# Optimization experiments

Measured on AMD Instinct MI355X. Metric: run time of the kernel, lower is better.

## Reference

```python
import jax, jax.numpy as jnp
import numpy as np

N_NODES = 100000
N_EDGES = 1600000
N_FEAT = 128
HID = 64


def setup_inputs() -> dict:
    key = jax.random.key(0)
    ks = jax.random.split(key, 8)
    s = 0.05
    return {
        "x": jax.random.normal(ks[0], (N_NODES, N_FEAT), jnp.float32),
        "edge_index": jax.random.randint(ks[1], (2, N_EDGES), 0, N_NODES, jnp.int64),
        "labels": jax.random.randint(ks[2], (N_NODES, 1), 0, 2, jnp.int32),
        "W1": jax.random.normal(ks[3], (N_FEAT, HID), jnp.float32) * s,
        "b1": jnp.zeros((HID,), jnp.float32),
        "W2": jax.random.normal(ks[4], (HID, HID), jnp.float32) * s,
        "b2": jnp.zeros((HID,), jnp.float32),
        "W3": jax.random.normal(ks[5], (HID, HID), jnp.float32) * s,
        "b3": jnp.zeros((HID,), jnp.float32),
        "lW1": jax.random.normal(ks[6], (HID, 8), jnp.float32) * s,
        "lb1": jnp.zeros((8,), jnp.float32),
        "lW2": jax.random.normal(ks[7], (8, 1), jnp.float32) * s,
        "lb2": jnp.zeros((1,), jnp.float32),
    }


def reference(x, edge_index, labels, W1, b1, W2, b2, W3, b3, lW1, lb1, lW2, lb2):
    n = x.shape[0]
    # PyG GCNConv: add self-loops, symmetric D^{-1/2}(A+I)D^{-1/2} normalization
    loop = jnp.arange(n)
    row = jnp.concatenate([edge_index[0], loop])  # sources
    col = jnp.concatenate([edge_index[1], loop])  # targets (aggregation)
    deg = jax.ops.segment_sum(jnp.ones(col.shape, x.dtype), col, num_segments=n)
    dinv = jax.lax.rsqrt(deg)  # deg >= 1 thanks to self loops
    norm = dinv[row] * dinv[col]  # [E+N]

    def gcn(h, W, b):
        m = (h @ W)[row] * norm[:, None]  # gather + scale per edge
        return jax.ops.segment_sum(m, col, num_segments=n) + b

    h = jax.nn.relu(gcn(x, W1, b1))   # dropout inactive in eval mode
    h = jax.nn.relu(gcn(h, W2, b2))
    h = jax.nn.relu(gcn(h, W3, b3))
    h = jax.nn.relu(h @ lW1 + lb1)
    p = jax.nn.sigmoid(h @ lW2 + lb2)  # [N,1]

    y = labels.astype(x.dtype)
    # generate_weights(labels): class-balance weights (minority class up-weighted)
    pm = jnp.mean(y)
    w = y * (1.0 - pm) + (1.0 - y) * pm
    eps = 1e-7
    pc = jnp.clip(p, eps, 1.0 - eps)
    bce = -(y * jnp.log(pc) + (1.0 - y) * jnp.log(1.0 - pc))
    loss = jnp.mean(w * bce)
    return loss, p
```

## Files before the change

### kernel.cpp

```cpp
#include <hip/hip_runtime.h>
#include <cstdint>
#include <cstddef>

typedef __attribute__((ext_vector_type(8))) short short8;
typedef __attribute__((ext_vector_type(4))) float f32x4;
typedef __attribute__((ext_vector_type(2))) float f32x2;

#define NBLK 512
#define NBLK_SHIFT 9

__device__ inline unsigned short f2bf(float f) {
  union { float f; unsigned int u; } x; x.f = f;
  unsigned int r = x.u + 0x7FFFu + ((x.u >> 16) & 1u);
  return (unsigned short)(r >> 16);
}
__device__ inline float bf2f(unsigned short s) {
  union { unsigned int u; float f; } x; x.u = ((unsigned int)s) << 16;
  return x.f;
}


__global__ __launch_bounds__(256) void hist_kernel(const int* __restrict__ cols,
                                                   int* __restrict__ histG,
                                                   const int* __restrict__ labels,
                                                   float* __restrict__ labelsum,
                                                   const float* __restrict__ W1,
                                                   const float* __restrict__ W2,
                                                   const float* __restrict__ W3,
                                                   unsigned short* __restrict__ Wt1,
                                                   unsigned short* __restrict__ Wt2,
                                                   unsigned short* __restrict__ Wt3,
                                                   int E, int N, int NBUCK) {
  __shared__ int h[512];
  if (blockIdx.x < 3) {
    const float* W; unsigned short* Wt; int K;
    if (blockIdx.x == 0)      { W = W1; Wt = Wt1; K = 128; }
    else if (blockIdx.x == 1) { W = W2; Wt = Wt2; K = 64; }
    else                      { W = W3; Wt = Wt3; K = 64; }
    int total = K * 64;
    for (int i = threadIdx.x; i < total; i += 256) {
      int n = i / K, k = i - n * K;
      Wt[i] = f2bf(W[k * 64 + n]);
    }
  }
  {
    int chunkL = (N + NBLK - 1) / NBLK;
    int ls = blockIdx.x * chunkL;
    int le = min(N, ls + chunkL);
    float v = 0.f;
    for (int i = ls + threadIdx.x; i < le; i += 256) v += (float)labels[i];
#pragma unroll
    for (int o = 32; o > 0; o >>= 1) v += __shfl_down(v, o);
    __shared__ float sl[4];
    if ((threadIdx.x & 63) == 0) sl[threadIdx.x >> 6] = v;
    __syncthreads();
    if (threadIdx.x == 0) labelsum[blockIdx.x] = sl[0] + sl[1] + sl[2] + sl[3];
  }
  for (int i = threadIdx.x; i < NBUCK; i += 256) h[i] = 0;
  __syncthreads();
  int chunk = (E + NBLK - 1) / NBLK;
  int s = blockIdx.x * chunk;
  int e = min(E, s + chunk);
  for (int i = s + threadIdx.x; i < e; i += 256) atomicAdd(&h[cols[i] >> 8], 1);
  __syncthreads();
  for (int i = threadIdx.x; i < NBUCK; i += 256)
    histG[blockIdx.x * NBUCK + i] = h[i];
}


__global__ __launch_bounds__(256) void scan_partials_t(const int* __restrict__ histG,
                                                       int* __restrict__ partials,
                                                       int total, int NBUCK) {
  int i = blockIdx.x * 256 + threadIdx.x;
  int v = 0;
  if (i < total) {
    int bucket = i >> NBLK_SHIFT, blk = i & (NBLK - 1);
    v = histG[blk * NBUCK + bucket];
  }
#pragma unroll
  for (int o = 32; o > 0; o >>= 1) v += __shfl_down(v, o);
  __shared__ int s[4];
  if ((threadIdx.x & 63) == 0) s[threadIdx.x >> 6] = v;
  __syncthreads();
  if (threadIdx.x == 0) partials[blockIdx.x] = s[0] + s[1] + s[2] + s[3];
}

__global__ __launch_bounds__(256) void scan_block(int* __restrict__ partials, int nb,
                                                  float* __restrict__ loss,
                                                  const float* __restrict__ labelsum,
                                                  float* __restrict__ pmsum) {
  __shared__ int tmp[256];
  __shared__ int carry;
  int tid = threadIdx.x;
  {
    float v = 0.f;
    for (int i = tid; i < NBLK; i += 256) v += labelsum[i];
#pragma unroll
    for (int o = 32; o > 0; o >>= 1) v += __shfl_down(v, o);
    __shared__ float sl[4];
    if ((tid & 63) == 0) sl[tid >> 6] = v;
    __syncthreads();
    if (tid == 0) *pmsum = sl[0] + sl[1] + sl[2] + sl[3];
  }
  if (tid == 0) { carry = 0; *loss = 0.f; }
  __syncthreads();
  for (int base = 0; base < nb; base += 256) {
    int i = base + tid;
    int v = (i < nb) ? partials[i] : 0;
    tmp[tid] = v;
    __syncthreads();
    int incl = v;
    for (int o = 1; o < 256; o <<= 1) {
      int t = (tid >= o) ? tmp[tid - o] : 0;
      __syncthreads();
      incl += t;
      tmp[tid] = incl;
      __syncthreads();
    }
    int total = tmp[255];
    int c = carry;
    if (i < nb) partials[i] = c + incl - v;
    __syncthreads();
    if (tid == 0) carry = c + total;
    __syncthreads();
  }
}

__global__ __launch_bounds__(256) void scan_final_t(const int* __restrict__ histG,
                                                    const int* __restrict__ partials,
                                                    int* __restrict__ scannedG,
                                                    int total, int NBUCK) {
  __shared__ int tmp[256];
  int tid = threadIdx.x;
  int i = blockIdx.x * 256 + tid;
  int bucket = i >> NBLK_SHIFT, blk = i & (NBLK - 1);
  int v = (i < total) ? histG[blk * NBUCK + bucket] : 0;
  tmp[tid] = v;
  __syncthreads();
  int incl = v;
  for (int o = 1; o < 256; o <<= 1) {
    int t = (tid >= o) ? tmp[tid - o] : 0;
    __syncthreads();
    incl += t;
    tmp[tid] = incl;
    __syncthreads();
  }
  if (i < total) scannedG[blk * NBUCK + bucket] = partials[blockIdx.x] + incl - v;
}


__global__ __launch_bounds__(256) void scatter_kernel(const int* __restrict__ rows,
                                                      const int* __restrict__ cols,
                                                      const int* __restrict__ scannedG,
                                                      unsigned int* __restrict__ packed,
                                                      int E, int NBUCK) {
  __shared__ int cur[512];
  for (int i = threadIdx.x; i < NBUCK; i += 256)
    cur[i] = scannedG[blockIdx.x * NBUCK + i];
  __syncthreads();
  int chunk = (E + NBLK - 1) / NBLK;
  int s = blockIdx.x * chunk;
  int e = min(E, s + chunk);
  for (int i = s + threadIdx.x; i < e; i += 256) {
    int c = cols[i];
    int r = rows[i];
    int pos = atomicAdd(&cur[c >> 8], 1);
    packed[pos] = ((unsigned int)(c & 255) << 24) | (unsigned int)r;
  }
}


__global__ __launch_bounds__(1024) void csr_finalize(const unsigned int* __restrict__ packed,
                                                     const int* __restrict__ scannedG,
                                                     int* __restrict__ sorted_src,
                                                     int* __restrict__ offsets,
                                                     float* __restrict__ dinv,
                                                     int N, int E, int NBUCK) {
  __shared__ int h[256];
  __shared__ int tmp[256];
  __shared__ int cur[256];
  int b = blockIdx.x;
  int tid = threadIdx.x;
  int base = scannedG[b];
  int end = (b + 1 < NBUCK) ? scannedG[b + 1] : E;
  if (tid < 256) h[tid] = 0;
  __syncthreads();
  for (int i = base + tid; i < end; i += 1024)
    atomicAdd(&h[packed[i] >> 24], 1);
  __syncthreads();
  if (tid < 256) {
    int v = h[tid];
    tmp[tid] = v;
  }
  __syncthreads();
  if (tid < 256) {
    int v = h[tid];
    int incl = v;
    for (int o = 1; o < 256; o <<= 1) {
      int t = (tid >= o) ? tmp[tid - o] : 0;
      __syncthreads();
      incl += t;
      tmp[tid] = incl;
      __syncthreads();
    }
    int excl = incl - v;
    int node = b * 256 + tid;
    if (node < N) {
      offsets[node] = base + excl;
      dinv[node] = rsqrtf((float)(v + 1));
    }
    cur[tid] = base + excl;
    if (b == NBUCK - 1 && tid == 0) offsets[N] = E;
  } else {
    for (int o = 1; o < 256; o <<= 1) { __syncthreads(); __syncthreads(); }
  }
  __syncthreads();
  for (int i = base + tid; i < end; i += 1024) {
    unsigned int p = packed[i];
    int pos = atomicAdd(&cur[p >> 24], 1);
    sorted_src[pos] = (int)(p & 0xFFFFFFu);
  }
}


__global__ __launch_bounds__(256) void mfma_gemm1(const float* __restrict__ xv,
                                                  const unsigned short* __restrict__ Wt,
                                                  const float* __restrict__ dinv,
                                                  unsigned char* __restrict__ out, int N) {
  const int K = 128;
  __shared__ unsigned short tile[4][16 * 68];
  int w = threadIdx.x >> 6, lane = threadIdx.x & 63;
  int m = lane & 15, quad = lane >> 4;
  int m0 = blockIdx.x * 64 + w * 16;
  int rowA = m0 + m;
  bool rowOK = rowA < N;
  f32x4 acc[4] = {{0.f,0.f,0.f,0.f},{0.f,0.f,0.f,0.f},{0.f,0.f,0.f,0.f},{0.f,0.f,0.f,0.f}};
#pragma unroll
  for (int kc = 0; kc < K / 32; ++kc) {
    short8 a = {0, 0, 0, 0, 0, 0, 0, 0};
    if (rowOK) {
      const float* hp = xv + (size_t)rowA * K + kc * 32 + quad * 8;
      float4 p0 = ((const float4*)hp)[0];
      float4 p1 = ((const float4*)hp)[1];
      a[0] = (short)f2bf(p0.x); a[1] = (short)f2bf(p0.y);
      a[2] = (short)f2bf(p0.z); a[3] = (short)f2bf(p0.w);
      a[4] = (short)f2bf(p1.x); a[5] = (short)f2bf(p1.y);
      a[6] = (short)f2bf(p1.z); a[7] = (short)f2bf(p1.w);
    }
#pragma unroll
    for (int t = 0; t < 4; ++t) {
      short8 b = *(const short8*)(Wt + (size_t)(t * 16 + m) * K + kc * 32 + quad * 8);
      acc[t] = __builtin_amdgcn_mfma_f32_16x16x32_bf16(a, b, acc[t], 0, 0, 0);
    }
  }
  unsigned short* tw = tile[w];
#pragma unroll
  for (int r = 0; r < 4; ++r) {
    int row = quad * 4 + r;
    int gr = m0 + row;
    float dv = dinv[gr < N ? gr : 0];
#pragma unroll
    for (int t = 0; t < 4; ++t)
      tw[row * 68 + t * 16 + m] = f2bf(acc[t][r] * dv);
  }
#pragma unroll
  for (int p = 0; p < 4; ++p) {
    int row = p * 4 + (lane >> 4);
    int ch = lane & 15;
    int gr = m0 + row;
    if (gr < N) {
      uint2 v = *(const uint2*)(tw + row * 68 + ch * 4);
      float f0 = bf2f((unsigned short)(v.x & 0xFFFFu));
      float f1 = bf2f((unsigned short)(v.x >> 16));
      float f2 = bf2f((unsigned short)(v.y & 0xFFFFu));
      float f3 = bf2f((unsigned short)(v.y >> 16));
      int pk = 0;
      pk = __builtin_amdgcn_cvt_pk_fp8_f32(f0, f1, pk, false);
      pk = __builtin_amdgcn_cvt_pk_fp8_f32(f2, f3, pk, true);
      *(unsigned int*)(out + (size_t)gr * 64 + ch * 4) = (unsigned int)pk;
    }
  }
}


__global__ __launch_bounds__(256) void agg_gemm(const unsigned char* __restrict__ A8in,
                                                const int* __restrict__ offsets,
                                                const int* __restrict__ sorted_src,
                                                const float* __restrict__ dinv,
                                                const float* __restrict__ bias,
                                                const unsigned short* __restrict__ Wt,
                                                unsigned char* __restrict__ A8out, int N) {
  __shared__ unsigned short hl[32 * 68];
  int cl = threadIdx.x >> 3;
  int c = blockIdx.x * 32 + cl;
  int l = threadIdx.x & 7;
  int obase = threadIdx.x & 56;
  bool ok = c < N;
  int s = 0, e = 0;
  float dc = 0.f;
  uint2 svr = {0u, 0u};
  if (ok) {
    s = offsets[c]; e = offsets[c + 1];
    dc = dinv[c];
    svr = *(const uint2*)(A8in + ((size_t)c << 6) + l * 8);
  }
  f32x2 a0 = {0.f, 0.f}, a1 = {0.f, 0.f}, a2 = {0.f, 0.f}, a3 = {0.f, 0.f};
  for (int base = s; base < e; base += 16) {
    int i0 = base + l, i1 = base + 8 + l;
    int r0 = (i0 < e) ? __builtin_nontemporal_load(sorted_src + i0) : 0;
    int r1 = (i1 < e) ? __builtin_nontemporal_load(sorted_src + i1) : 0;
    int cnt = e - base; if (cnt > 16) cnt = 16;
    int rj[16];
#pragma unroll
    for (int t = 0; t < 8; ++t)  rj[t] = __shfl(r0, obase + t);
#pragma unroll
    for (int t = 8; t < 16; ++t) rj[t] = __shfl(r1, obase + (t - 8));
#pragma unroll
    for (int t = 0; t < 16; ++t) {
      if (t < cnt) {
        uint2 v = *(const uint2*)(A8in + ((size_t)(unsigned int)rj[t] << 6) + l * 8);
        a0 += __builtin_amdgcn_cvt_pk_f32_fp8((int)v.x, false);
        a1 += __builtin_amdgcn_cvt_pk_f32_fp8((int)v.x, true);
        a2 += __builtin_amdgcn_cvt_pk_f32_fp8((int)v.y, false);
        a3 += __builtin_amdgcn_cvt_pk_f32_fp8((int)v.y, true);
      }
    }
  }
  {
    f32x2 s0 = __builtin_amdgcn_cvt_pk_f32_fp8((int)svr.x, false);
    f32x2 s1 = __builtin_amdgcn_cvt_pk_f32_fp8((int)svr.x, true);
    f32x2 s2 = __builtin_amdgcn_cvt_pk_f32_fp8((int)svr.y, false);
    f32x2 s3 = __builtin_amdgcn_cvt_pk_f32_fp8((int)svr.y, true);
    float acc[8] = {a0[0] + s0[0], a0[1] + s0[1], a1[0] + s1[0], a1[1] + s1[1],
                    a2[0] + s2[0], a2[1] + s2[1], a3[0] + s3[0], a3[1] + s3[1]};
    const float* bp = bias + l * 8;
    unsigned int w0 = 0, w1 = 0, w2 = 0, w3 = 0;
    if (ok) {
      unsigned short hv[8];
#pragma unroll
      for (int q = 0; q < 8; ++q) {
        float v = fmaf(acc[q], dc, bp[q]);
        hv[q] = f2bf(v > 0.f ? v : 0.f);
      }
      w0 = (unsigned int)hv[0] | ((unsigned int)hv[1] << 16);
      w1 = (unsigned int)hv[2] | ((unsigned int)hv[3] << 16);
      w2 = (unsigned int)hv[4] | ((unsigned int)hv[5] << 16);
      w3 = (unsigned int)hv[6] | ((unsigned int)hv[7] << 16);
    }
    unsigned int* dst = (unsigned int*)(hl + cl * 68 + l * 8);
    dst[0] = w0; dst[1] = w1; dst[2] = w2; dst[3] = w3;
  }
  __syncthreads();
  int wv = threadIdx.x >> 6, lane = threadIdx.x & 63;
  int m = lane & 15, quad = lane >> 4;
  int rbase = (wv & 1) * 16, cbase = (wv >> 1) * 32;
  f32x4 acc2[2] = {{0.f,0.f,0.f,0.f},{0.f,0.f,0.f,0.f}};
#pragma unroll
  for (int kc = 0; kc < 2; ++kc) {
    union { uint2 u[2]; short8 s8; } av;
    const unsigned int* ap = (const unsigned int*)(hl + (rbase + m) * 68 + kc * 32 + quad * 8);
    av.u[0] = ((const uint2*)ap)[0];
    av.u[1] = ((const uint2*)ap)[1];
#pragma unroll
    for (int t = 0; t < 2; ++t) {
      short8 b = *(const short8*)(Wt + (size_t)(cbase + t * 16 + m) * 64 + kc * 32 + quad * 8);
      acc2[t] = __builtin_amdgcn_mfma_f32_16x16x32_bf16(av.s8, b, acc2[t], 0, 0, 0);
    }
  }
  __syncthreads();
#pragma unroll
  for (int r = 0; r < 4; ++r) {
    int row = rbase + quad * 4 + r;
    int gr = blockIdx.x * 32 + row;
    float dv = dinv[gr < N ? gr : 0];
#pragma unroll
    for (int t = 0; t < 2; ++t)
      hl[row * 68 + cbase + t * 16 + m] = f2bf(acc2[t][r] * dv);
  }
  __syncthreads();
#pragma unroll
  for (int u = 0; u < 2; ++u) {
    int id = threadIdx.x * 2 + u;
    int row = id >> 4, ch = id & 15;
    int gr = blockIdx.x * 32 + row;
    if (gr < N) {
      uint2 v = *(const uint2*)(hl + row * 68 + ch * 4);
      float f0 = bf2f((unsigned short)(v.x & 0xFFFFu));
      float f1 = bf2f((unsigned short)(v.x >> 16));
      float f2 = bf2f((unsigned short)(v.y & 0xFFFFu));
      float f3 = bf2f((unsigned short)(v.y >> 16));
      int pk = 0;
      pk = __builtin_amdgcn_cvt_pk_fp8_f32(f0, f1, pk, false);
      pk = __builtin_amdgcn_cvt_pk_fp8_f32(f2, f3, pk, true);
      *(unsigned int*)(A8out + (size_t)gr * 64 + ch * 4) = (unsigned int)pk;
    }
  }
}


__global__ __launch_bounds__(256) void agg_head(const unsigned char* __restrict__ A8in,
                                                const int* __restrict__ offsets,
                                                const int* __restrict__ sorted_src,
                                                const float* __restrict__ dinv,
                                                const float* __restrict__ bias,
                                                const float* __restrict__ lW1,
                                                const float* __restrict__ lb1,
                                                const float* __restrict__ lW2,
                                                const float* __restrict__ lb2,
                                                const int* __restrict__ labels,
                                                const float* __restrict__ pmsum,
                                                float* __restrict__ p,
                                                float* __restrict__ loss, int N) {
  int cl = threadIdx.x >> 3;
  int c = blockIdx.x * 32 + cl;
  int l = threadIdx.x & 7;
  int obase = threadIdx.x & 56;
  bool ok = c < N;
  int s = 0, e = 0;
  float dc = 0.f;
  uint2 svr = {0u, 0u};
  if (ok) {
    s = offsets[c]; e = offsets[c + 1];
    dc = dinv[c];
    svr = *(const uint2*)(A8in + ((size_t)c << 6) + l * 8);
  }
  f32x2 a0 = {0.f, 0.f}, a1 = {0.f, 0.f}, a2 = {0.f, 0.f}, a3 = {0.f, 0.f};
  for (int base = s; base < e; base += 16) {
    int i0 = base + l, i1 = base + 8 + l;
    int r0 = (i0 < e) ? __builtin_nontemporal_load(sorted_src + i0) : 0;
    int r1 = (i1 < e) ? __builtin_nontemporal_load(sorted_src + i1) : 0;
    int cnt = e - base; if (cnt > 16) cnt = 16;
    int rj[16];
#pragma unroll
    for (int t = 0; t < 8; ++t)  rj[t] = __shfl(r0, obase + t);
#pragma unroll
    for (int t = 8; t < 16; ++t) rj[t] = __shfl(r1, obase + (t - 8));
#pragma unroll
    for (int t = 0; t < 16; ++t) {
      if (t < cnt) {
        uint2 v = *(const uint2*)(A8in + ((size_t)(unsigned int)rj[t] << 6) + l * 8);
        a0 += __builtin_amdgcn_cvt_pk_f32_fp8((int)v.x, false);
        a1 += __builtin_amdgcn_cvt_pk_f32_fp8((int)v.x, true);
        a2 += __builtin_amdgcn_cvt_pk_f32_fp8((int)v.y, false);
        a3 += __builtin_amdgcn_cvt_pk_f32_fp8((int)v.y, true);
      }
    }
  }
  float contrib = 0.f;
  {
    f32x2 s0 = __builtin_amdgcn_cvt_pk_f32_fp8((int)svr.x, false);
    f32x2 s1 = __builtin_amdgcn_cvt_pk_f32_fp8((int)svr.x, true);
    f32x2 s2 = __builtin_amdgcn_cvt_pk_f32_fp8((int)svr.y, false);
    f32x2 s3 = __builtin_amdgcn_cvt_pk_f32_fp8((int)svr.y, true);
    float acc[8] = {a0[0] + s0[0], a0[1] + s0[1], a1[0] + s1[0], a1[1] + s1[1],
                    a2[0] + s2[0], a2[1] + s2[1], a3[0] + s3[0], a3[1] + s3[1]};
    const float* bp = bias + l * 8;
    float hq[8];
#pragma unroll
    for (int q = 0; q < 8; ++q) {
      float v = fmaf(acc[q], dc, bp[q]);
      hq[q] = v > 0.f ? v : 0.f;
    }
    float acc8[8] = {0.f,0.f,0.f,0.f,0.f,0.f,0.f,0.f};
#pragma unroll
    for (int q = 0; q < 8; ++q) {
      int k = l * 8 + q;
#pragma unroll
      for (int j = 0; j < 8; ++j) acc8[j] = fmaf(hq[q], lW1[k * 8 + j], acc8[j]);
    }
#pragma unroll
    for (int j = 0; j < 8; ++j) {
      acc8[j] += __shfl_xor(acc8[j], 1);
      acc8[j] += __shfl_xor(acc8[j], 2);
      acc8[j] += __shfl_xor(acc8[j], 4);
    }
    if (ok && l == 0) {
      float sv = lb2[0];
#pragma unroll
      for (int j = 0; j < 8; ++j) {
        float a = acc8[j] + lb1[j];
        a = a > 0.f ? a : 0.f;
        sv = fmaf(a, lW2[j], sv);
      }
      float pv = 1.0f / (1.0f + expf(-sv));
      p[c] = pv;
      float pm = *pmsum / (float)N;
      float y = (float)labels[c];
      float w = y * (1.f - pm) + (1.f - y) * pm;
      float pc = fminf(fmaxf(pv, 1e-7f), 1.f - 1e-7f);
      float bce = -(y * logf(pc) + (1.f - y) * logf(1.f - pc));
      contrib = w * bce / (float)N;
    }
  }
#pragma unroll
  for (int o = 32; o > 0; o >>= 1) contrib += __shfl_down(contrib, o);
  __shared__ float sh[4];
  int lane = threadIdx.x & 63, wv = threadIdx.x >> 6;
  if (lane == 0) sh[wv] = contrib;
  __syncthreads();
  if (threadIdx.x == 0) atomicAdd(loss, sh[0] + sh[1] + sh[2] + sh[3]);
}


extern "C" void kernel_launch(void* const* d_in, const int* in_sizes, int n_in,
                              void* d_out, int out_size, void* d_ws, size_t ws_size,
                              hipStream_t stream) {
  const float* x      = (const float*)d_in[0];
  const int*   ei     = (const int*)d_in[1];
  const int*   labels = (const int*)d_in[2];
  const float* W1 = (const float*)d_in[3];
  const float* b1 = (const float*)d_in[4];
  const float* W2 = (const float*)d_in[5];
  const float* b2 = (const float*)d_in[6];
  const float* W3 = (const float*)d_in[7];
  const float* b3 = (const float*)d_in[8];
  const float* lW1 = (const float*)d_in[9];
  const float* lb1 = (const float*)d_in[10];
  const float* lW2 = (const float*)d_in[11];
  const float* lb2 = (const float*)d_in[12];

  int N = in_sizes[2];
  int E = in_sizes[1] / 2;
  const int* rows = ei;
  const int* cols = ei + E;

  int Npad = (N + 63) & ~63;
  int NBUCK = (N + 255) >> 8;
  int totalH = NBUCK * NBLK;
  int nb2 = (totalH + 255) / 256;

  char* ws = (char*)d_ws;
  unsigned char*  A8a = (unsigned char*)ws;
  unsigned char*  A8b = (unsigned char*)(ws + (size_t)Npad * 64);
  unsigned short* Wt1 = (unsigned short*)(ws + (size_t)Npad * 192);
  unsigned short* Wt2 = Wt1 + 64 * 128;
  unsigned short* Wt3 = Wt2 + 64 * 64;
  float* dinv     = (float*)(Wt3 + 64 * 64);
  int*   offsets  = (int*)(dinv + N);
  int*   histG    = offsets + N + 1;
  int*   scanned  = histG + totalH;
  unsigned int* packed = (unsigned int*)(scanned + totalH);
  int*   sorted   = (int*)(packed + E);
  int*   partials = sorted + E;
  float* pmsum    = (float*)(partials + nb2);
  float* labelsum = pmsum + 1;

  float* loss = (float*)d_out;
  float* p    = (float*)d_out + 1;

  int gemmBlocks = Npad / 64;
  int aggBlocks  = (N + 31) / 32;

  hist_kernel<<<NBLK, 256, 0, stream>>>(cols, histG, labels, labelsum,
                                        W1, W2, W3, Wt1, Wt2, Wt3, E, N, NBUCK);
  scan_partials_t<<<nb2, 256, 0, stream>>>(histG, partials, totalH, NBUCK);
  scan_block<<<1, 256, 0, stream>>>(partials, nb2, loss, labelsum, pmsum);
  scan_final_t<<<nb2, 256, 0, stream>>>(histG, partials, scanned, totalH, NBUCK);
  scatter_kernel<<<NBLK, 256, 0, stream>>>(rows, cols, scanned, packed, E, NBUCK);
  csr_finalize<<<NBUCK, 1024, 0, stream>>>(packed, scanned, sorted, offsets, dinv, N, E, NBUCK);

  mfma_gemm1<<<gemmBlocks, 256, 0, stream>>>(x, Wt1, dinv, A8a, N);

  agg_gemm<<<aggBlocks, 256, 0, stream>>>(A8a, offsets, sorted, dinv, b1, Wt2, A8b, N);
  agg_gemm<<<aggBlocks, 256, 0, stream>>>(A8b, offsets, sorted, dinv, b2, Wt3, A8a, N);
  agg_head<<<aggBlocks, 256, 0, stream>>>(A8a, offsets, sorted, dinv, b3,
                                          lW1, lb1, lW2, lb2, labels, pmsum, p, loss, N);
}
```

Before: 329.0 us.

## Use 4 lanes per node with 16-byte gathers in aggregation kernels

The aggregation kernels now assign 4 threads per destination node instead of 8, with each lane gathering 16 fp8 features through 128-bit loads. Each block therefore covers 64 nodes, and each wave computes a full 16x64 MFMA tile. The aim is fewer, wider memory transactions per neighbor row and fewer blocks to launch. The trade-off is more accumulator registers per thread and half the thread-level parallelism per node, which could hurt latency hiding on the irregular gathers.

```diff
diff --git a/kernel.cpp b/kernel.cpp
--- a/kernel.cpp
+++ b/kernel.cpp
@@ -283,6 +283,41 @@
 }
 
 
+#define GATHER_CORE(A8in)                                                        \
+  f32x2 a0={0.f,0.f},a1={0.f,0.f},a2={0.f,0.f},a3={0.f,0.f};                     \
+  f32x2 a4={0.f,0.f},a5={0.f,0.f},a6={0.f,0.f},a7={0.f,0.f};                     \
+  for (int base = s; base < e; base += 16) {                                     \
+    int i0 = base + l4 * 4;                                                      \
+    int r0 = (i0     < e) ? __builtin_nontemporal_load(sorted_src + i0)     : 0; \
+    int r1 = (i0 + 1 < e) ? __builtin_nontemporal_load(sorted_src + i0 + 1) : 0; \
+    int r2 = (i0 + 2 < e) ? __builtin_nontemporal_load(sorted_src + i0 + 2) : 0; \
+    int r3 = (i0 + 3 < e) ? __builtin_nontemporal_load(sorted_src + i0 + 3) : 0; \
+    int cnt = e - base; if (cnt > 16) cnt = 16;                                  \
+    int rj[16];                                                                  \
+    _Pragma("unroll")                                                            \
+    for (int s4 = 0; s4 < 4; ++s4) {                                             \
+      rj[s4 * 4 + 0] = __shfl(r0, qbase + s4);                                   \
+      rj[s4 * 4 + 1] = __shfl(r1, qbase + s4);                                   \
+      rj[s4 * 4 + 2] = __shfl(r2, qbase + s4);                                   \
+      rj[s4 * 4 + 3] = __shfl(r3, qbase + s4);                                   \
+    }                                                                            \
+    _Pragma("unroll")                                                            \
+    for (int t = 0; t < 16; ++t) {                                               \
+      if (t < cnt) {                                                             \
+        uint4 v = *(const uint4*)(A8in + ((size_t)(unsigned int)rj[t] << 6) + l4 * 16); \
+        a0 += __builtin_amdgcn_cvt_pk_f32_fp8((int)v.x, false);                  \
+        a1 += __builtin_amdgcn_cvt_pk_f32_fp8((int)v.x, true);                   \
+        a2 += __builtin_amdgcn_cvt_pk_f32_fp8((int)v.y, false);                  \
+        a3 += __builtin_amdgcn_cvt_pk_f32_fp8((int)v.y, true);                   \
+        a4 += __builtin_amdgcn_cvt_pk_f32_fp8((int)v.z, false);                  \
+        a5 += __builtin_amdgcn_cvt_pk_f32_fp8((int)v.z, true);                   \
+        a6 += __builtin_amdgcn_cvt_pk_f32_fp8((int)v.w, false);                  \
+        a7 += __builtin_amdgcn_cvt_pk_f32_fp8((int)v.w, true);                   \
+      }                                                                          \
+    }                                                                            \
+  }
+
+
 __global__ __launch_bounds__(256) void agg_gemm(const unsigned char* __restrict__ A8in,
                                                 const int* __restrict__ offsets,
                                                 const int* __restrict__ sorted_src,
@@ -290,101 +325,82 @@
                                                 const float* __restrict__ bias,
                                                 const unsigned short* __restrict__ Wt,
                                                 unsigned char* __restrict__ A8out, int N) {
-  __shared__ unsigned short hl[32 * 68];
-  int cl = threadIdx.x >> 3;
-  int c = blockIdx.x * 32 + cl;
-  int l = threadIdx.x & 7;
-  int obase = threadIdx.x & 56;
+  __shared__ unsigned short hl[64 * 72];
+  int lane = threadIdx.x & 63;
+  int cl = threadIdx.x >> 2;
+  int c = blockIdx.x * 64 + cl;
+  int l4 = lane & 3;
+  int qbase = lane & 60;
   bool ok = c < N;
   int s = 0, e = 0;
   float dc = 0.f;
-  uint2 svr = {0u, 0u};
+  uint4 svr = {0u, 0u, 0u, 0u};
   if (ok) {
     s = offsets[c]; e = offsets[c + 1];
     dc = dinv[c];
-    svr = *(const uint2*)(A8in + ((size_t)c << 6) + l * 8);
-  }
-  f32x2 a0 = {0.f, 0.f}, a1 = {0.f, 0.f}, a2 = {0.f, 0.f}, a3 = {0.f, 0.f};
-  for (int base = s; base < e; base += 16) {
-    int i0 = base + l, i1 = base + 8 + l;
-    int r0 = (i0 < e) ? __builtin_nontemporal_load(sorted_src + i0) : 0;
-    int r1 = (i1 < e) ? __builtin_nontemporal_load(sorted_src + i1) : 0;
-    int cnt = e - base; if (cnt > 16) cnt = 16;
-    int rj[16];
-#pragma unroll
-    for (int t = 0; t < 8; ++t)  rj[t] = __shfl(r0, obase + t);
-#pragma unroll
-    for (int t = 8; t < 16; ++t) rj[t] = __shfl(r1, obase + (t - 8));
-#pragma unroll
-    for (int t = 0; t < 16; ++t) {
-      if (t < cnt) {
-        uint2 v = *(const uint2*)(A8in + ((size_t)(unsigned int)rj[t] << 6) + l * 8);
-        a0 += __builtin_amdgcn_cvt_pk_f32_fp8((int)v.x, false);
-        a1 += __builtin_amdgcn_cvt_pk_f32_fp8((int)v.x, true);
-        a2 += __builtin_amdgcn_cvt_pk_f32_fp8((int)v.y, false);
-        a3 += __builtin_amdgcn_cvt_pk_f32_fp8((int)v.y, true);
+    svr = *(const uint4*)(A8in + ((size_t)c << 6) + l4 * 16);
+  }
+  GATHER_CORE(A8in)
+  {
+    short8 w0 = {0,0,0,0,0,0,0,0}, w1 = {0,0,0,0,0,0,0,0};
+    if (ok) {
+      a0 += __builtin_amdgcn_cvt_pk_f32_fp8((int)svr.x, false);
+      a1 += __builtin_amdgcn_cvt_pk_f32_fp8((int)svr.x, true);
+      a2 += __builtin_amdgcn_cvt_pk_f32_fp8((int)svr.y, false);
+      a3 += __builtin_amdgcn_cvt_pk_f32_fp8((int)svr.y, true);
+      a4 += __builtin_amdgcn_cvt_pk_f32_fp8((int)svr.z, false);
+      a5 += __builtin_amdgcn_cvt_pk_f32_fp8((int)svr.z, true);
+      a6 += __builtin_amdgcn_cvt_pk_f32_fp8((int)svr.w, false);
+      a7 += __builtin_amdgcn_cvt_pk_f32_fp8((int)svr.w, true);
+      float accf[16] = {a0[0],a0[1],a1[0],a1[1],a2[0],a2[1],a3[0],a3[1],
+                        a4[0],a4[1],a5[0],a5[1],a6[0],a6[1],a7[0],a7[1]};
+      const float* bp = bias + l4 * 16;
+#pragma unroll
+      for (int q = 0; q < 8; ++q) {
+        float v = fmaf(accf[q], dc, bp[q]);
+        w0[q] = (short)f2bf(v > 0.f ? v : 0.f);
       }
-    }
-  }
-  {
-    f32x2 s0 = __builtin_amdgcn_cvt_pk_f32_fp8((int)svr.x, false);
-    f32x2 s1 = __builtin_amdgcn_cvt_pk_f32_fp8((int)svr.x, true);
-    f32x2 s2 = __builtin_amdgcn_cvt_pk_f32_fp8((int)svr.y, false);
-    f32x2 s3 = __builtin_amdgcn_cvt_pk_f32_fp8((int)svr.y, true);
-    float acc[8] = {a0[0] + s0[0], a0[1] + s0[1], a1[0] + s1[0], a1[1] + s1[1],
-                    a2[0] + s2[0], a2[1] + s2[1], a3[0] + s3[0], a3[1] + s3[1]};
-    const float* bp = bias + l * 8;
-    unsigned int w0 = 0, w1 = 0, w2 = 0, w3 = 0;
-    if (ok) {
-      unsigned short hv[8];
 #pragma unroll
       for (int q = 0; q < 8; ++q) {
-        float v = fmaf(acc[q], dc, bp[q]);
-        hv[q] = f2bf(v > 0.f ? v : 0.f);
+        float v = fmaf(accf[8 + q], dc, bp[8 + q]);
+        w1[q] = (short)f2bf(v > 0.f ? v : 0.f);
       }
-      w0 = (unsigned int)hv[0] | ((unsigned int)hv[1] << 16);
-      w1 = (unsigned int)hv[2] | ((unsigned int)hv[3] << 16);
-      w2 = (unsigned int)hv[4] | ((unsigned int)hv[5] << 16);
-      w3 = (unsigned int)hv[6] | ((unsigned int)hv[7] << 16);
-    }
-    unsigned int* dst = (unsigned int*)(hl + cl * 68 + l * 8);
-    dst[0] = w0; dst[1] = w1; dst[2] = w2; dst[3] = w3;
-  }
-  __syncthreads();
-  int wv = threadIdx.x >> 6, lane = threadIdx.x & 63;
+    }
+    short8* dst = (short8*)(hl + cl * 72 + l4 * 16);
+    dst[0] = w0; dst[1] = w1;
+  }
+  __syncthreads();
+  int wv = threadIdx.x >> 6;
   int m = lane & 15, quad = lane >> 4;
-  int rbase = (wv & 1) * 16, cbase = (wv >> 1) * 32;
-  f32x4 acc2[2] = {{0.f,0.f,0.f,0.f},{0.f,0.f,0.f,0.f}};
+  int rbase = wv * 16;
+  f32x4 acc2[4] = {{0.f,0.f,0.f,0.f},{0.f,0.f,0.f,0.f},{0.f,0.f,0.f,0.f},{0.f,0.f,0.f,0.f}};
 #pragma unroll
   for (int kc = 0; kc < 2; ++kc) {
-    union { uint2 u[2]; short8 s8; } av;
-    const unsigned int* ap = (const unsigned int*)(hl + (rbase + m) * 68 + kc * 32 + quad * 8);
-    av.u[0] = ((const uint2*)ap)[0];
-    av.u[1] = ((const uint2*)ap)[1];
-#pragma unroll
-    for (int t = 0; t < 2; ++t) {
-      short8 b = *(const short8*)(Wt + (size_t)(cbase + t * 16 + m) * 64 + kc * 32 + quad * 8);
-      acc2[t] = __builtin_amdgcn_mfma_f32_16x16x32_bf16(av.s8, b, acc2[t], 0, 0, 0);
+    short8 a = *(const short8*)(hl + (rbase + m) * 72 + kc * 32 + quad * 8);
+#pragma unroll
+    for (int t = 0; t < 4; ++t) {
+      short8 b = *(const short8*)(Wt + (size_t)(t * 16 + m) * 64 + kc * 32 + quad * 8);
+      acc2[t] = __builtin_amdgcn_mfma_f32_16x16x32_bf16(a, b, acc2[t], 0, 0, 0);
     }
   }
   __syncthreads();
 #pragma unroll
   for (int r = 0; r < 4; ++r) {
     int row = rbase + quad * 4 + r;
-    int gr = blockIdx.x * 32 + row;
+    int gr = blockIdx.x * 64 + row;
     float dv = dinv[gr < N ? gr : 0];
 #pragma unroll
-    for (int t = 0; t < 2; ++t)
-      hl[row * 68 + cbase + t * 16 + m] = f2bf(acc2[t][r] * dv);
-  }
-  __syncthreads();
-#pragma unroll
-  for (int u = 0; u < 2; ++u) {
-    int id = threadIdx.x * 2 + u;
+    for (int t = 0; t < 4; ++t)
+      hl[row * 72 + t * 16 + m] = f2bf(acc2[t][r] * dv);
+  }
+  __syncthreads();
+#pragma unroll
+  for (int u = 0; u < 4; ++u) {
+    int id = u * 256 + threadIdx.x;
     int row = id >> 4, ch = id & 15;
-    int gr = blockIdx.x * 32 + row;
+    int gr = blockIdx.x * 64 + row;
     if (gr < N) {
-      uint2 v = *(const uint2*)(hl + row * 68 + ch * 4);
+      uint2 v = *(const uint2*)(hl + row * 72 + ch * 4);
       float f0 = bf2f((unsigned short)(v.x & 0xFFFFu));
       float f1 = bf2f((unsigned short)(v.x >> 16));
       float f2 = bf2f((unsigned short)(v.y & 0xFFFFu));
@@ -411,60 +427,44 @@
                                                 const float* __restrict__ pmsum,
                                                 float* __restrict__ p,
                                                 float* __restrict__ loss, int N) {
-  int cl = threadIdx.x >> 3;
-  int c = blockIdx.x * 32 + cl;
-  int l = threadIdx.x & 7;
-  int obase = threadIdx.x & 56;
+  int lane = threadIdx.x & 63;
+  int cl = threadIdx.x >> 2;
+  int c = blockIdx.x * 64 + cl;
+  int l4 = lane & 3;
+  int qbase = lane & 60;
   bool ok = c < N;
   int s = 0, e = 0;
   float dc = 0.f;
-  uint2 svr = {0u, 0u};
+  uint4 svr = {0u, 0u, 0u, 0u};
   if (ok) {
     s = offsets[c]; e = offsets[c + 1];
     dc = dinv[c];
-    svr = *(const uint2*)(A8in + ((size_t)c << 6) + l * 8);
-  }
-  f32x2 a0 = {0.f, 0.f}, a1 = {0.f, 0.f}, a2 = {0.f, 0.f}, a3 = {0.f, 0.f};
-  for (int base = s; base < e; base += 16) {
-    int i0 = base + l, i1 = base + 8 + l;
-    int r0 = (i0 < e) ? __builtin_nontemporal_load(sorted_src + i0) : 0;
-    int r1 = (i1 < e) ? __builtin_nontemporal_load(sorted_src + i1) : 0;
-    int cnt = e - base; if (cnt > 16) cnt = 16;
-    int rj[16];
-#pragma unroll
-    for (int t = 0; t < 8; ++t)  rj[t] = __shfl(r0, obase + t);
-#pragma unroll
-    for (int t = 8; t < 16; ++t) rj[t] = __shfl(r1, obase + (t - 8));
-#pragma unroll
-    for (int t = 0; t < 16; ++t) {
-      if (t < cnt) {
-        uint2 v = *(const uint2*)(A8in + ((size_t)(unsigned int)rj[t] << 6) + l * 8);
-        a0 += __builtin_amdgcn_cvt_pk_f32_fp8((int)v.x, false);
-        a1 += __builtin_amdgcn_cvt_pk_f32_fp8((int)v.x, true);
-        a2 += __builtin_amdgcn_cvt_pk_f32_fp8((int)v.y, false);
-        a3 += __builtin_amdgcn_cvt_pk_f32_fp8((int)v.y, true);
-      }
-    }
-  }
+    svr = *(const uint4*)(A8in + ((size_t)c << 6) + l4 * 16);
+  }
+  GATHER_CORE(A8in)
   float contrib = 0.f;
   {
-    f32x2 s0 = __builtin_amdgcn_cvt_pk_f32_fp8((int)svr.x, false);
-    f32x2 s1 = __builtin_amdgcn_cvt_pk_f32_fp8((int)svr.x, true);
-    f32x2 s2 = __builtin_amdgcn_cvt_pk_f32_fp8((int)svr.y, false);
-    f32x2 s3 = __builtin_amdgcn_cvt_pk_f32_fp8((int)svr.y, true);
-    float acc[8] = {a0[0] + s0[0], a0[1] + s0[1], a1[0] + s1[0], a1[1] + s1[1],
-                    a2[0] + s2[0], a2[1] + s2[1], a3[0] + s3[0], a3[1] + s3[1]};
-    const float* bp = bias + l * 8;
-    float hq[8];
-#pragma unroll
-    for (int q = 0; q < 8; ++q) {
-      float v = fmaf(acc[q], dc, bp[q]);
+    a0 += __builtin_amdgcn_cvt_pk_f32_fp8((int)svr.x, false);
+    a1 += __builtin_amdgcn_cvt_pk_f32_fp8((int)svr.x, true);
+    a2 += __builtin_amdgcn_cvt_pk_f32_fp8((int)svr.y, false);
+    a3 += __builtin_amdgcn_cvt_pk_f32_fp8((int)svr.y, true);
+    a4 += __builtin_amdgcn_cvt_pk_f32_fp8((int)svr.z, false);
+    a5 += __builtin_amdgcn_cvt_pk_f32_fp8((int)svr.z, true);
+    a6 += __builtin_amdgcn_cvt_pk_f32_fp8((int)svr.w, false);
+    a7 += __builtin_amdgcn_cvt_pk_f32_fp8((int)svr.w, true);
+    float accf[16] = {a0[0],a0[1],a1[0],a1[1],a2[0],a2[1],a3[0],a3[1],
+                      a4[0],a4[1],a5[0],a5[1],a6[0],a6[1],a7[0],a7[1]};
+    const float* bp = bias + l4 * 16;
+    float hq[16];
+#pragma unroll
+    for (int q = 0; q < 16; ++q) {
+      float v = fmaf(accf[q], dc, bp[q]);
       hq[q] = v > 0.f ? v : 0.f;
     }
     float acc8[8] = {0.f,0.f,0.f,0.f,0.f,0.f,0.f,0.f};
 #pragma unroll
-    for (int q = 0; q < 8; ++q) {
-      int k = l * 8 + q;
+    for (int q = 0; q < 16; ++q) {
+      int k = l4 * 16 + q;
 #pragma unroll
       for (int j = 0; j < 8; ++j) acc8[j] = fmaf(hq[q], lW1[k * 8 + j], acc8[j]);
     }
@@ -472,9 +472,8 @@
     for (int j = 0; j < 8; ++j) {
       acc8[j] += __shfl_xor(acc8[j], 1);
       acc8[j] += __shfl_xor(acc8[j], 2);
-      acc8[j] += __shfl_xor(acc8[j], 4);
-    }
-    if (ok && l == 0) {
+    }
+    if (ok && l4 == 0) {
       float sv = lb2[0];
 #pragma unroll
       for (int j = 0; j < 8; ++j) {
@@ -495,7 +494,7 @@
 #pragma unroll
   for (int o = 32; o > 0; o >>= 1) contrib += __shfl_down(contrib, o);
   __shared__ float sh[4];
-  int lane = threadIdx.x & 63, wv = threadIdx.x >> 6;
+  int wv = threadIdx.x >> 6;
   if (lane == 0) sh[wv] = contrib;
   __syncthreads();
   if (threadIdx.x == 0) atomicAdd(loss, sh[0] + sh[1] + sh[2] + sh[3]);
@@ -549,7 +548,7 @@
   float* p    = (float*)d_out + 1;
 
   int gemmBlocks = Npad / 64;
-  int aggBlocks  = (N + 31) / 32;
+  int aggBlocks  = (N + 63) / 64;
 
   hist_kernel<<<NBLK, 256, 0, stream>>>(cols, histG, labels, labelsum,
                                         W1, W2, W3, Wt1, Wt2, Wt3, E, N, NBUCK);
```

Measured after the change: 306.0 us. 1.08x faster.
